# Optimization experiments

Measured on AMD Instinct MI355X. Metric: run time of the kernel, lower is better.

Reference implementation:

```python
import jax, jax.numpy as jnp
import numpy as np

L, B, IN, H, OUT = 4, 4096, 1024, 1024, 1024


def setup_inputs() -> dict:
    key = jax.random.key(0)
    ks = jax.random.split(key, 9)
    std = 1.0 / (H + IN) ** 0.5
    return {
        "x": jax.random.normal(ks[0], (B, IN), jnp.float32),
        "h_prev": jax.random.normal(ks[1], (L, B, H), jnp.float32),
        "c_prev": jax.random.normal(ks[2], (L, B, H), jnp.float32),
        "Wi": jax.random.uniform(ks[3], (L, IN, 4 * H), jnp.float32, -std, std),
        "Wh": jax.random.uniform(ks[4], (L, H, 4 * H), jnp.float32, -std, std),
        "bi": jax.random.uniform(ks[5], (L, 4 * H), jnp.float32, -std, std),
        "bh": jax.random.uniform(ks[6], (L, 4 * H), jnp.float32, -std, std),
        "fc_W": jax.random.uniform(ks[7], (H, OUT), jnp.float32, -std, std),
        "fc_b": jax.random.uniform(ks[8], (OUT,), jnp.float32, -std, std),
    }


def _lstm_cell(x, h, c, Wi, Wh, bi, bh):
    # gates: [B, 4H], split into (input, forget, cell, output)
    gates = x @ Wi + bi + h @ Wh + bh
    i, f, g, o = jnp.split(gates, 4, axis=1)
    i, f, o = jax.nn.sigmoid(i), jax.nn.sigmoid(f), jax.nn.sigmoid(o)
    g = jnp.tanh(g)
    c_cur = f * c + i * g
    h_cur = o * jnp.tanh(c_cur)
    return h_cur, c_cur


def reference(x, h_prev, c_prev, Wi, Wh, bi, bh, fc_W, fc_b):
    h_out, c_out = [], []
    x_in = x
    for l in range(L):  # fixed small layer loop
        h_cur, c_cur = _lstm_cell(x_in, h_prev[l], c_prev[l], Wi[l], Wh[l], bi[l], bh[l])
        h_out.append(h_cur)
        c_out.append(c_cur)
        x_in = h_cur
    h_out = jnp.stack(h_out, axis=0)
    c_out = jnp.stack(c_out, axis=0)
    y = h_out[-1] @ fc_W + fc_b
    return y, h_out, c_out
```

## Files before the change

### kernel.cpp

```cpp
#include <hip/hip_runtime.h>

#define B_    4096
#define H_    1024
#define NLAY  4
#define NT512 512

typedef __attribute__((ext_vector_type(8))) short bf16x8;
typedef __attribute__((ext_vector_type(4))) short s16x4;
typedef __attribute__((ext_vector_type(4))) float f32x4;
typedef unsigned short ushort_t;

__device__ __forceinline__ ushort_t f2bf(float f) {
  unsigned u = __builtin_bit_cast(unsigned, f);
  u += 0x7FFFu + ((u >> 16) & 1u);
  return (ushort_t)(u >> 16);
}

__device__ __forceinline__ float fast_sigmoid(float x) {
  float e = __expf(-fabsf(x));
  float s = 1.0f / (1.0f + e);
  return x >= 0.0f ? s : 1.0f - s;
}
__device__ __forceinline__ float fast_tanh(float x) {
  float e = __expf(-2.0f * fabsf(x));
  float t = (1.0f - e) / (1.0f + e);
  return x >= 0.0f ? t : -t;
}

#define GLDS16(gsrc, ldst)                                                  \
  __builtin_amdgcn_global_load_lds(                                         \
      (__attribute__((address_space(1))) void*)(gsrc),                      \
      (__attribute__((address_space(3))) void*)(ldst), 16, 0, 0)

#define BAR()                                                               \
  { asm volatile("" ::: "memory");                                          \
    __builtin_amdgcn_s_barrier();                                           \
    asm volatile("" ::: "memory"); }

#define WAITV(N)                                                            \
  { asm volatile("s_waitcnt vmcnt(" #N ")" ::: "memory");                   \
    __builtin_amdgcn_sched_barrier(0); }

__global__ __launch_bounds__(NT512, 2) void lstm8(
    const ushort_t* __restrict__ aX, const ushort_t* __restrict__ aH,
    const float* __restrict__ cprev, const float* __restrict__ bi,
    const float* __restrict__ bh, const ushort_t* __restrict__ wt,
    float* __restrict__ hout, float* __restrict__ cout,
    ushort_t* __restrict__ hbfout) {
  __shared__ __align__(16) char sL[131072];

  const int tid  = threadIdx.x;
  const int lane = tid & 63;
  const int wid  = tid >> 6;
  const int wm   = wid >> 2;
  const int wn   = wid & 3;
  const int bid  = (blockIdx.x & 7) * 32 + (blockIdx.x >> 3);
  const int bm   = bid & 15;
  const int bn   = bid >> 4;

  const int fr    = lane & 15;
  const int oF    = lane >> 4;
  const int s_    = oF ^ ((fr >> 1) & 3);
  const int aBase = (wm * 128 + fr) * 64 + s_ * 16;
  const int bBase = (wn * 64 + fr) * 64 + s_ * 16;

  const int rA = tid >> 2;
  const int oA = (tid & 3) ^ ((rA >> 1) & 3);
  const size_t aOff = (size_t)(bm * 256 + rA) * 1024 + oA * 8;

  const ushort_t* wtBn = wt + (size_t)bn * 64 * 8192;

  f32x4 acc[8][4];
#pragma unroll
  for (int m = 0; m < 8; ++m)
#pragma unroll
    for (int g = 0; g < 4; ++g) acc[m][g] = (f32x4){0.f, 0.f, 0.f, 0.f};

#pragma unroll
  for (int t = 0; t < 3; ++t) {
    const ushort_t* s0 = aX + aOff + t * 32;
    GLDS16(s0,          sL + t * 32768 + wid * 1024);
    GLDS16(s0 + 131072, sL + t * 32768 + 8192 + wid * 1024);
    const ushort_t* sb = wtBn + (size_t)t * 8192 + tid * 8;
    GLDS16(sb,        sL + t * 32768 + 16384 + wid * 1024);
    GLDS16(sb + 4096, sL + t * 32768 + 16384 + 8192 + wid * 1024);
  }
  WAITV(8);
  BAR();

#define TSTEP(BUFC, T, ISSUE)                                                \
  {                                                                          \
    const char* pa = sL + (BUFC) * 32768;                                    \
    const char* pb = pa + 16384;                                             \
    char* nbuf = sL + (((BUFC) + 3) & 3) * 32768;                            \
    bf16x8 a[8], b0, b1;                                                     \
    _Pragma("unroll")                                                        \
    for (int m = 0; m < 8; ++m)                                              \
      a[m] = *(const bf16x8*)(pa + aBase + m * 1024);                        \
    b0 = *(const bf16x8*)(pb + bBase);                                       \
    b1 = *(const bf16x8*)(pb + bBase + 1024);                                \
    if (ISSUE) {                                                             \
      const int tt = (T) + 3;                                                \
      const ushort_t* s0 = (tt < 32 ? aX : aH) + (aOff + (tt & 31) * 32);    \
      GLDS16(s0,          nbuf + wid * 1024);                                \
      GLDS16(s0 + 131072, nbuf + 8192 + wid * 1024);                         \
    }                                                                        \
    __builtin_amdgcn_s_setprio(1);                                           \
    _Pragma("unroll")                                                        \
    for (int m = 0; m < 8; ++m)                                              \
      acc[m][0] =                                                            \
          __builtin_amdgcn_mfma_f32_16x16x32_bf16(a[m], b0, acc[m][0], 0, 0, 0); \
    _Pragma("unroll")                                                        \
    for (int m = 0; m < 8; ++m)                                              \
      acc[m][1] =                                                            \
          __builtin_amdgcn_mfma_f32_16x16x32_bf16(a[m], b1, acc[m][1], 0, 0, 0); \
    __builtin_amdgcn_s_setprio(0);                                           \
    bf16x8 b2 = *(const bf16x8*)(pb + bBase + 2048);                         \
    bf16x8 b3 = *(const bf16x8*)(pb + bBase + 3072);                         \
    if (ISSUE) {                                                             \
      const int tt = (T) + 3;                                                \
      const ushort_t* sb = wtBn + (size_t)tt * 8192 + tid * 8;               \
      GLDS16(sb,        nbuf + 16384 + wid * 1024);                          \
      GLDS16(sb + 4096, nbuf + 16384 + 8192 + wid * 1024);                   \
    }                                                                        \
    __builtin_amdgcn_s_setprio(1);                                           \
    _Pragma("unroll")                                                        \
    for (int m = 0; m < 8; ++m)                                              \
      acc[m][2] =                                                            \
          __builtin_amdgcn_mfma_f32_16x16x32_bf16(a[m], b2, acc[m][2], 0, 0, 0); \
    _Pragma("unroll")                                                        \
    for (int m = 0; m < 8; ++m)                                              \
      acc[m][3] =                                                            \
          __builtin_amdgcn_mfma_f32_16x16x32_bf16(a[m], b3, acc[m][3], 0, 0, 0); \
    __builtin_amdgcn_s_setprio(0);                                           \
  }

#pragma unroll 1
  for (int t = 0; t < 60; t += 4) {
    TSTEP(0, t + 0, 1) WAITV(8); BAR();
    TSTEP(1, t + 1, 1) WAITV(8); BAR();
    TSTEP(2, t + 2, 1) WAITV(8); BAR();
    TSTEP(3, t + 3, 1) WAITV(8); BAR();
  }
  TSTEP(0, 60, 1) WAITV(8); BAR();
  TSTEP(1, 61, 0) WAITV(4); BAR();
  TSTEP(2, 62, 0) WAITV(0); BAR();
  TSTEP(3, 63, 0)
#undef TSTEP

  const int hcolL = wn * 16 + fr;
  const int hcol  = bn * 64 + hcolL;
  float bsum[4];
#pragma unroll
  for (int g = 0; g < 4; ++g)
    bsum[g] = bi[g * 1024 + hcol] + bh[g * 1024 + hcol];

#define LSTRIDE 68
  float* LF = (float*)sL;
  const int crow = (tid >> 4);
  const int cc4  = (tid & 15) * 4;
  BAR();
  {
    const float* cp0 = cprev + (size_t)(bm * 256) * 1024 + bn * 64;
#pragma unroll
    for (int i = 0; i < 8; ++i) {
      const int row = i * 32 + crow;
      f32x4 v = *(const f32x4*)(cp0 + (size_t)row * 1024 + cc4);
      *(f32x4*)(LF + row * LSTRIDE + cc4) = v;
    }
  }
  BAR();
  float cv[8][4], hv[8][4];
#pragma unroll
  for (int m = 0; m < 8; ++m) {
    const int rowb = wm * 128 + m * 16 + oF * 4;
#pragma unroll
    for (int r = 0; r < 4; ++r) {
      const float cp = LF[(rowb + r) * LSTRIDE + hcolL];
      const float gi = fast_sigmoid(acc[m][0][r] + bsum[0]);
      const float gf = fast_sigmoid(acc[m][1][r] + bsum[1]);
      const float gg = fast_tanh(acc[m][2][r] + bsum[2]);
      const float go = fast_sigmoid(acc[m][3][r] + bsum[3]);
      const float c  = gf * cp + gi * gg;
      cv[m][r] = c;
      hv[m][r] = go * fast_tanh(c);
    }
  }
  BAR();
#pragma unroll
  for (int m = 0; m < 8; ++m) {
    const int rowb = wm * 128 + m * 16 + oF * 4;
#pragma unroll
    for (int r = 0; r < 4; ++r) LF[(rowb + r) * LSTRIDE + hcolL] = cv[m][r];
  }
  BAR();
  {
    float* co0 = cout + (size_t)(bm * 256) * 1024 + bn * 64;
#pragma unroll
    for (int i = 0; i < 8; ++i) {
      const int row = i * 32 + crow;
      f32x4 v = *(const f32x4*)(LF + row * LSTRIDE + cc4);
      *(f32x4*)(co0 + (size_t)row * 1024 + cc4) = v;
    }
  }
  BAR();
#pragma unroll
  for (int m = 0; m < 8; ++m) {
    const int rowb = wm * 128 + m * 16 + oF * 4;
#pragma unroll
    for (int r = 0; r < 4; ++r) LF[(rowb + r) * LSTRIDE + hcolL] = hv[m][r];
  }
  BAR();
  {
    float* ho0 = hout + (size_t)(bm * 256) * 1024 + bn * 64;
    ushort_t* hb0 = hbfout + (size_t)(bm * 256) * 1024 + bn * 64;
#pragma unroll
    for (int i = 0; i < 8; ++i) {
      const int row = i * 32 + crow;
      f32x4 v = *(const f32x4*)(LF + row * LSTRIDE + cc4);
      *(f32x4*)(ho0 + (size_t)row * 1024 + cc4) = v;
      s16x4 hb;
#pragma unroll
      for (int j = 0; j < 4; ++j) hb[j] = (short)f2bf(v[j]);
      *(s16x4*)(hb0 + (size_t)row * 1024 + cc4) = hb;
    }
  }
#undef LSTRIDE
}

__global__ __launch_bounds__(NT512) void packW(const float* __restrict__ Wi,
                                               const float* __restrict__ Wh,
                                               ushort_t* __restrict__ wt) {
  __shared__ ushort_t t16[64 * 256];
  const int bn = blockIdx.x;
  const int kb = blockIdx.y;
  const int l  = blockIdx.z;
  const int tid = threadIdx.x;
  const int kq = tid >> 6, cc = tid & 63;
  const int k0 = kb * 64;
  const float* W = (k0 < 1024)
                       ? (Wi + (size_t)l * 1024 * 4096 + (size_t)k0 * 4096)
                       : (Wh + (size_t)l * 1024 * 4096 + (size_t)(k0 - 1024) * 4096);
#pragma unroll
  for (int kk = 0; kk < 8; ++kk) {
    const int kl = kq * 8 + kk;
#pragma unroll
    for (int g = 0; g < 4; ++g) {
      const float v = W[(size_t)kl * 4096 + g * 1024 + bn * 64 + cc];
      const int p = (cc >> 4) * 64 + g * 16 + (cc & 15);
      t16[kl * 256 + p] = f2bf(v);
    }
  }
  __syncthreads();
#pragma unroll
  for (int half = 0; half < 2; ++half) {
    ushort_t* tile =
        wt + (((size_t)l * 16 + bn) * 64 + kb * 2 + half) * 8192;
#pragma unroll
    for (int j = 0; j < 2; ++j) {
      const int q = j * 512 + tid;
      const int r = q >> 2, s = q & 3;
      const int o = s ^ ((r >> 1) & 3);
      const int kl = half * 32 + o * 8;
      bf16x8 ov;
#pragma unroll
      for (int i = 0; i < 8; ++i) ov[i] = (short)t16[(kl + i) * 256 + r];
      *(bf16x8*)(tile + (size_t)q * 8) = ov;
    }
  }
}

__device__ __forceinline__ int swz(int row, int kelem) {
  return ((row * 64 + kelem) * 2) ^ ((row & 7) << 4);
}

__global__ __launch_bounds__(NT512) void fc_kernel(
    const ushort_t* __restrict__ wtfc, const ushort_t* __restrict__ abf,
    const float* __restrict__ bias, float* __restrict__ y) {
  __shared__ __align__(16) char sA[128 * 64 * 2];
  __shared__ __align__(16) char sB[64 * 64 * 2];
  const int tid  = threadIdx.x;
  const int lane = tid & 63;
  const int wid  = tid >> 6;
  const int wm   = wid >> 2;
  const int wn   = wid & 3;
  const int bid  = (blockIdx.x & 7) * 64 + (blockIdx.x >> 3);
  const int bm   = bid & 31;
  const int bn   = bid >> 5;

  f32x4 acc[4];
#pragma unroll
  for (int m = 0; m < 4; ++m) acc[m] = (f32x4){0.f, 0.f, 0.f, 0.f};

  const int rloc = wid * 8 + (lane >> 3);
  const int jA   = (lane & 7) ^ ((lane >> 3) & 7);
  const ushort_t* aSrc = abf + (size_t)(bm * 128 + rloc) * 1024 + jA * 8;

  for (int ks = 0; ks < 16; ++ks) {
    __syncthreads();
    GLDS16(wtfc + (size_t)(bn * 16 + ks) * 4096 + tid * 8, sB + wid * 1024);
    const int off = ks * 64;
    GLDS16(aSrc + off,             sA + wid * 1024);
    GLDS16(aSrc + off + 64 * 1024, sA + 8192 + wid * 1024);
    __syncthreads();
#pragma unroll
    for (int kk = 0; kk < 64; kk += 32) {
      const int ke = kk + (lane >> 4) * 8;
      bf16x8 a[4];
#pragma unroll
      for (int m = 0; m < 4; ++m)
        a[m] = *(const bf16x8*)(sA + swz(wm * 64 + m * 16 + (lane & 15), ke));
      bf16x8 b = *(const bf16x8*)(sB + swz(wn * 16 + (lane & 15), ke));
#pragma unroll
      for (int m = 0; m < 4; ++m)
        acc[m] = __builtin_amdgcn_mfma_f32_16x16x32_bf16(a[m], b, acc[m], 0, 0, 0);
    }
  }
  const int col = bn * 64 + wn * 16 + (lane & 15);
  const float bb = bias[col];
#pragma unroll
  for (int m = 0; m < 4; ++m) {
    const int row0 = bm * 128 + wm * 64 + m * 16 + ((lane >> 4) << 2);
#pragma unroll
    for (int r = 0; r < 4; ++r)
      y[(size_t)(row0 + r) * 1024 + col] = acc[m][r] + bb;
  }
}

__global__ __launch_bounds__(NT512) void transposeFc(const float* __restrict__ W,
                                                     ushort_t* __restrict__ wt) {
  const int bn = blockIdx.x;
  const int ks = blockIdx.y;
  const int tid = threadIdx.x;
  const int c  = tid & 63;
  const int ko = (tid >> 6) * 8;
  float v[8];
#pragma unroll
  for (int j = 0; j < 8; ++j)
    v[j] = W[(size_t)(ks * 64 + ko + j) * 1024 + bn * 64 + c];
  bf16x8 o;
#pragma unroll
  for (int j = 0; j < 8; ++j) o[j] = (short)f2bf(v[j]);
  ushort_t* tile = wt + ((size_t)bn * 16 + ks) * 4096;
  *(bf16x8*)((char*)tile + swz(c, ko)) = o;
}

__global__ __launch_bounds__(256) void cvt_bf16(const float* __restrict__ s,
                                                ushort_t* __restrict__ d,
                                                int n8) {
  const int i = blockIdx.x * 256 + threadIdx.x;
  if (i >= n8) return;
  const float* p = s + (size_t)i * 8;
  f32x4 a = ((const f32x4*)p)[0];
  f32x4 b = ((const f32x4*)p)[1];
  bf16x8 o;
#pragma unroll
  for (int j = 0; j < 4; ++j) {
    o[j]     = (short)f2bf(a[j]);
    o[4 + j] = (short)f2bf(b[j]);
  }
  *(bf16x8*)(d + (size_t)i * 8) = o;
}

extern "C" void kernel_launch(void* const* d_in, const int* in_sizes, int n_in,
                              void* d_out, int out_size, void* d_ws,
                              size_t ws_size, hipStream_t stream) {
  const float* x     = (const float*)d_in[0];
  const float* hprev = (const float*)d_in[1];
  const float* cprev = (const float*)d_in[2];
  const float* Wi    = (const float*)d_in[3];
  const float* Wh    = (const float*)d_in[4];
  const float* bi    = (const float*)d_in[5];
  const float* bh    = (const float*)d_in[6];
  const float* fcW   = (const float*)d_in[7];
  const float* fcb   = (const float*)d_in[8];

  float* out = (float*)d_out;
  const size_t BH = (size_t)B_ * H_;
  float* y    = out;
  float* hout = out + BH;
  float* cout = out + 5 * BH;

  const size_t WT_ELEMS = (size_t)4 * 16 * 64 * 8192;
  const size_t FC_ELEMS = (size_t)16 * 16 * 4096;
  ushort_t* wt      = (ushort_t*)d_ws;
  ushort_t* fcwt    = wt + WT_ELEMS;
  ushort_t* xbf     = fcwt + FC_ELEMS;
  ushort_t* hprevbf = xbf + BH;
  ushort_t* houtbf  = hprevbf + 4 * BH;

  dim3 blk(NT512);
  packW<<<dim3(16, 32, 4), blk, 0, stream>>>(Wi, Wh, wt);
  transposeFc<<<dim3(16, 16), blk, 0, stream>>>(fcW, fcwt);
  cvt_bf16<<<dim3((int)(BH / 8 / 256)), dim3(256), 0, stream>>>(x, xbf,
                                                                (int)(BH / 8));
  cvt_bf16<<<dim3((int)(4 * BH / 8 / 256)), dim3(256), 0, stream>>>(
      hprev, hprevbf, (int)(4 * BH / 8));

  for (int l = 0; l < NLAY; ++l) {
    const ushort_t* aX  = (l == 0) ? xbf : (houtbf + (size_t)(l - 1) * BH);
    const ushort_t* wtl = wt + (size_t)l * 16 * 64 * 8192;
    lstm8<<<dim3(256), blk, 0, stream>>>(
        aX, hprevbf + (size_t)l * BH, cprev + (size_t)l * BH, bi + l * 4096,
        bh + l * 4096, wtl, hout + (size_t)l * BH, cout + (size_t)l * BH,
        houtbf + (size_t)l * BH);
  }
  fc_kernel<<<dim3(512), blk, 0, stream>>>(fcwt, houtbf + 3 * BH, fcb, y);
}
```

Measured before the change: 391.6 us.

## Shrink LSTM GEMM tile and stream weight fragments directly into registers

Each LSTM block now runs 256 threads on a 128x64 output tile instead of 512 threads on 256x64, and launches 512 blocks. Shared memory per block drops from 128KB to 32KB. Only the activation tile is staged through LDS; each wave loads its weight fragments straight from global memory into registers, double-buffered two steps ahead, and packW is changed to lay out weights in MFMA-lane order for this. The aim is higher occupancy and less LDS traffic and capacity pressure, at the cost of less A-tile reuse across column tiles and more register use for the prefetched B fragments.

```diff
diff --git a/kernel.cpp b/kernel.cpp
--- a/kernel.cpp
+++ b/kernel.cpp
@@ -3,7 +3,6 @@
 #define B_    4096
 #define H_    1024
 #define NLAY  4
-#define NT512 512
 
 typedef __attribute__((ext_vector_type(8))) short bf16x8;
 typedef __attribute__((ext_vector_type(4))) short s16x4;
@@ -41,34 +40,30 @@
   { asm volatile("s_waitcnt vmcnt(" #N ")" ::: "memory");                   \
     __builtin_amdgcn_sched_barrier(0); }
 
-__global__ __launch_bounds__(NT512, 2) void lstm8(
+__global__ __launch_bounds__(256, 2) void lstm8(
     const ushort_t* __restrict__ aX, const ushort_t* __restrict__ aH,
     const float* __restrict__ cprev, const float* __restrict__ bi,
-    const float* __restrict__ bh, const ushort_t* __restrict__ wt,
+    const float* __restrict__ bh, const ushort_t* __restrict__ wtl,
     float* __restrict__ hout, float* __restrict__ cout,
     ushort_t* __restrict__ hbfout) {
-  __shared__ __align__(16) char sL[131072];
+  __shared__ __align__(16) char sL[32768];
 
   const int tid  = threadIdx.x;
   const int lane = tid & 63;
   const int wid  = tid >> 6;
-  const int wm   = wid >> 2;
-  const int wn   = wid & 3;
-  const int bid  = (blockIdx.x & 7) * 32 + (blockIdx.x >> 3);
-  const int bm   = bid & 15;
-  const int bn   = bid >> 4;
-
-  const int fr    = lane & 15;
-  const int oF    = lane >> 4;
-  const int s_    = oF ^ ((fr >> 1) & 3);
-  const int aBase = (wm * 128 + fr) * 64 + s_ * 16;
-  const int bBase = (wn * 64 + fr) * 64 + s_ * 16;
-
-  const int rA = tid >> 2;
-  const int oA = (tid & 3) ^ ((rA >> 1) & 3);
-  const size_t aOff = (size_t)(bm * 256 + rA) * 1024 + oA * 8;
-
-  const ushort_t* wtBn = wt + (size_t)bn * 64 * 8192;
+  const int bid  = (blockIdx.x & 7) * 64 + (blockIdx.x >> 3);
+  const int bm   = bid & 31;
+  const int bn   = bid >> 5;
+
+  const int fr = lane & 15;
+  const int oF = lane >> 4;
+  const int aBase = fr * 64 + (oF ^ ((fr >> 1) & 3)) * 16;
+
+  const int rowA = tid >> 2;
+  const int oA   = (tid & 3) ^ ((rowA >> 1) & 3);
+  const size_t aOff = (size_t)(bm * 128 + rowA) * 1024 + oA * 8;
+
+  const ushort_t* wtBn = wtl + (size_t)bn * 524288;
 
   f32x4 acc[8][4];
 #pragma unroll
@@ -76,107 +71,105 @@
 #pragma unroll
     for (int g = 0; g < 4; ++g) acc[m][g] = (f32x4){0.f, 0.f, 0.f, 0.f};
 
-#pragma unroll
-  for (int t = 0; t < 3; ++t) {
-    const ushort_t* s0 = aX + aOff + t * 32;
-    GLDS16(s0,          sL + t * 32768 + wid * 1024);
-    GLDS16(s0 + 131072, sL + t * 32768 + 8192 + wid * 1024);
-    const ushort_t* sb = wtBn + (size_t)t * 8192 + tid * 8;
-    GLDS16(sb,        sL + t * 32768 + 16384 + wid * 1024);
-    GLDS16(sb + 4096, sL + t * 32768 + 16384 + 8192 + wid * 1024);
-  }
-  WAITV(8);
-  BAR();
-
-#define TSTEP(BUFC, T, ISSUE)                                                \
+  bf16x8 bs0[4], bs1[4], bs2[4], bs3[4];
+
+#define STAGE_A(NB, T)                                                       \
   {                                                                          \
-    const char* pa = sL + (BUFC) * 32768;                                    \
-    const char* pb = pa + 16384;                                             \
-    char* nbuf = sL + (((BUFC) + 3) & 3) * 32768;                            \
-    bf16x8 a[8], b0, b1;                                                     \
+    const ushort_t* s0 = (((T) < 32) ? aX : aH) + aOff + ((T) & 31) * 32;    \
+    GLDS16(s0,         sL + (NB) * 8192 + wid * 1024);                       \
+    GLDS16(s0 + 65536, sL + (NB) * 8192 + 4096 + wid * 1024);                \
+  }
+#define LOADB(SET, T)                                                        \
+  {                                                                          \
+    const ushort_t* b0 =                                                     \
+        wtBn + ((size_t)(T) * 16 + wid * 4) * 512 + lane * 8;                \
+    SET[0] = *(const bf16x8*)(b0);                                           \
+    SET[1] = *(const bf16x8*)(b0 + 512);                                     \
+    SET[2] = *(const bf16x8*)(b0 + 1024);                                    \
+    SET[3] = *(const bf16x8*)(b0 + 1536);                                    \
+  }
+
+  STAGE_A(0, 0)
+  LOADB(bs0, 0)
+  STAGE_A(1, 1)
+  LOADB(bs1, 1)
+  STAGE_A(2, 2)
+  WAITV(8)
+  BAR()
+
+#define TSTEP(CB, NB, T, BU, BL, IB, IA)                                     \
+  {                                                                          \
+    const char* pa = sL + (CB) * 8192;                                       \
+    bf16x8 a[4];                                                             \
     _Pragma("unroll")                                                        \
-    for (int m = 0; m < 8; ++m)                                              \
+    for (int m = 0; m < 4; ++m)                                              \
       a[m] = *(const bf16x8*)(pa + aBase + m * 1024);                        \
-    b0 = *(const bf16x8*)(pb + bBase);                                       \
-    b1 = *(const bf16x8*)(pb + bBase + 1024);                                \
-    if (ISSUE) {                                                             \
-      const int tt = (T) + 3;                                                \
-      const ushort_t* s0 = (tt < 32 ? aX : aH) + (aOff + (tt & 31) * 32);    \
-      GLDS16(s0,          nbuf + wid * 1024);                                \
-      GLDS16(s0 + 131072, nbuf + 8192 + wid * 1024);                         \
-    }                                                                        \
+    if (IB) LOADB(BL, (T) + 2)                                               \
     __builtin_amdgcn_s_setprio(1);                                           \
     _Pragma("unroll")                                                        \
-    for (int m = 0; m < 8; ++m)                                              \
-      acc[m][0] =                                                            \
-          __builtin_amdgcn_mfma_f32_16x16x32_bf16(a[m], b0, acc[m][0], 0, 0, 0); \
+    for (int g = 0; g < 4; ++g)                                              \
+      _Pragma("unroll")                                                      \
+      for (int m = 0; m < 4; ++m)                                            \
+        acc[m][g] = __builtin_amdgcn_mfma_f32_16x16x32_bf16(a[m], BU[g],     \
+                                                            acc[m][g], 0, 0, 0); \
+    __builtin_amdgcn_s_setprio(0);                                           \
     _Pragma("unroll")                                                        \
-    for (int m = 0; m < 8; ++m)                                              \
-      acc[m][1] =                                                            \
-          __builtin_amdgcn_mfma_f32_16x16x32_bf16(a[m], b1, acc[m][1], 0, 0, 0); \
-    __builtin_amdgcn_s_setprio(0);                                           \
-    bf16x8 b2 = *(const bf16x8*)(pb + bBase + 2048);                         \
-    bf16x8 b3 = *(const bf16x8*)(pb + bBase + 3072);                         \
-    if (ISSUE) {                                                             \
-      const int tt = (T) + 3;                                                \
-      const ushort_t* sb = wtBn + (size_t)tt * 8192 + tid * 8;               \
-      GLDS16(sb,        nbuf + 16384 + wid * 1024);                          \
-      GLDS16(sb + 4096, nbuf + 16384 + 8192 + wid * 1024);                   \
-    }                                                                        \
+    for (int m = 0; m < 4; ++m)                                              \
+      a[m] = *(const bf16x8*)(pa + aBase + 4096 + m * 1024);                 \
+    if (IA) STAGE_A(NB, (T) + 3)                                             \
     __builtin_amdgcn_s_setprio(1);                                           \
     _Pragma("unroll")                                                        \
-    for (int m = 0; m < 8; ++m)                                              \
-      acc[m][2] =                                                            \
-          __builtin_amdgcn_mfma_f32_16x16x32_bf16(a[m], b2, acc[m][2], 0, 0, 0); \
-    _Pragma("unroll")                                                        \
-    for (int m = 0; m < 8; ++m)                                              \
-      acc[m][3] =                                                            \
-          __builtin_amdgcn_mfma_f32_16x16x32_bf16(a[m], b3, acc[m][3], 0, 0, 0); \
+    for (int g = 0; g < 4; ++g)                                              \
+      _Pragma("unroll")                                                      \
+      for (int m = 0; m < 4; ++m)                                            \
+        acc[m + 4][g] = __builtin_amdgcn_mfma_f32_16x16x32_bf16(              \
+            a[m], BU[g], acc[m + 4][g], 0, 0, 0);                            \
     __builtin_amdgcn_s_setprio(0);                                           \
   }
 
 #pragma unroll 1
   for (int t = 0; t < 60; t += 4) {
-    TSTEP(0, t + 0, 1) WAITV(8); BAR();
-    TSTEP(1, t + 1, 1) WAITV(8); BAR();
-    TSTEP(2, t + 2, 1) WAITV(8); BAR();
-    TSTEP(3, t + 3, 1) WAITV(8); BAR();
-  }
-  TSTEP(0, 60, 1) WAITV(8); BAR();
-  TSTEP(1, 61, 0) WAITV(4); BAR();
-  TSTEP(2, 62, 0) WAITV(0); BAR();
-  TSTEP(3, 63, 0)
+    TSTEP(0, 3, t + 0, bs0, bs2, 1, 1) WAITV(8) BAR()
+    TSTEP(1, 0, t + 1, bs1, bs3, 1, 1) WAITV(8) BAR()
+    TSTEP(2, 1, t + 2, bs2, bs0, 1, 1) WAITV(8) BAR()
+    TSTEP(3, 2, t + 3, bs3, bs1, 1, 1) WAITV(8) BAR()
+  }
+  TSTEP(0, 3, 60, bs0, bs2, 1, 1) WAITV(8) BAR()
+  TSTEP(1, 0, 61, bs1, bs3, 1, 0) WAITV(6) BAR()
+  TSTEP(2, 1, 62, bs2, bs0, 0, 0) WAITV(0) BAR()
+  TSTEP(3, 2, 63, bs3, bs0, 0, 0)
 #undef TSTEP
-
-  const int hcolL = wn * 16 + fr;
+#undef STAGE_A
+#undef LOADB
+
+  const int hcolL = wid * 16 + fr;
   const int hcol  = bn * 64 + hcolL;
   float bsum[4];
 #pragma unroll
   for (int g = 0; g < 4; ++g)
     bsum[g] = bi[g * 1024 + hcol] + bh[g * 1024 + hcol];
 
-#define LSTRIDE 68
   float* LF = (float*)sL;
-  const int crow = (tid >> 4);
+  const int crow = tid >> 4;
   const int cc4  = (tid & 15) * 4;
-  BAR();
+  BAR()
   {
-    const float* cp0 = cprev + (size_t)(bm * 256) * 1024 + bn * 64;
+    const float* cp0 = cprev + (size_t)(bm * 128) * 1024 + bn * 64;
 #pragma unroll
     for (int i = 0; i < 8; ++i) {
-      const int row = i * 32 + crow;
+      const int row = i * 16 + crow;
       f32x4 v = *(const f32x4*)(cp0 + (size_t)row * 1024 + cc4);
-      *(f32x4*)(LF + row * LSTRIDE + cc4) = v;
-    }
-  }
-  BAR();
+      *(f32x4*)(LF + row * 64 + cc4) = v;
+    }
+  }
+  BAR()
   float cv[8][4], hv[8][4];
 #pragma unroll
   for (int m = 0; m < 8; ++m) {
-    const int rowb = wm * 128 + m * 16 + oF * 4;
+    const int rowb = m * 16 + oF * 4;
 #pragma unroll
     for (int r = 0; r < 4; ++r) {
-      const float cp = LF[(rowb + r) * LSTRIDE + hcolL];
+      const float cp = LF[(rowb + r) * 64 + hcolL];
       const float gi = fast_sigmoid(acc[m][0][r] + bsum[0]);
       const float gf = fast_sigmoid(acc[m][1][r] + bsum[1]);
       const float gg = fast_tanh(acc[m][2][r] + bsum[2]);
@@ -186,38 +179,38 @@
       hv[m][r] = go * fast_tanh(c);
     }
   }
-  BAR();
+  BAR()
 #pragma unroll
   for (int m = 0; m < 8; ++m) {
-    const int rowb = wm * 128 + m * 16 + oF * 4;
-#pragma unroll
-    for (int r = 0; r < 4; ++r) LF[(rowb + r) * LSTRIDE + hcolL] = cv[m][r];
-  }
-  BAR();
+    const int rowb = m * 16 + oF * 4;
+#pragma unroll
+    for (int r = 0; r < 4; ++r) LF[(rowb + r) * 64 + hcolL] = cv[m][r];
+  }
+  BAR()
   {
-    float* co0 = cout + (size_t)(bm * 256) * 1024 + bn * 64;
+    float* co0 = cout + (size_t)(bm * 128) * 1024 + bn * 64;
 #pragma unroll
     for (int i = 0; i < 8; ++i) {
-      const int row = i * 32 + crow;
-      f32x4 v = *(const f32x4*)(LF + row * LSTRIDE + cc4);
+      const int row = i * 16 + crow;
+      f32x4 v = *(const f32x4*)(LF + row * 64 + cc4);
       *(f32x4*)(co0 + (size_t)row * 1024 + cc4) = v;
     }
   }
-  BAR();
+  BAR()
 #pragma unroll
   for (int m = 0; m < 8; ++m) {
-    const int rowb = wm * 128 + m * 16 + oF * 4;
-#pragma unroll
-    for (int r = 0; r < 4; ++r) LF[(rowb + r) * LSTRIDE + hcolL] = hv[m][r];
-  }
-  BAR();
+    const int rowb = m * 16 + oF * 4;
+#pragma unroll
+    for (int r = 0; r < 4; ++r) LF[(rowb + r) * 64 + hcolL] = hv[m][r];
+  }
+  BAR()
   {
-    float* ho0 = hout + (size_t)(bm * 256) * 1024 + bn * 64;
-    ushort_t* hb0 = hbfout + (size_t)(bm * 256) * 1024 + bn * 64;
+    float* ho0 = hout + (size_t)(bm * 128) * 1024 + bn * 64;
+    ushort_t* hb0 = hbfout + (size_t)(bm * 128) * 1024 + bn * 64;
 #pragma unroll
     for (int i = 0; i < 8; ++i) {
-      const int row = i * 32 + crow;
-      f32x4 v = *(const f32x4*)(LF + row * LSTRIDE + cc4);
+      const int row = i * 16 + crow;
+      f32x4 v = *(const f32x4*)(LF + row * 64 + cc4);
       *(f32x4*)(ho0 + (size_t)row * 1024 + cc4) = v;
       s16x4 hb;
 #pragma unroll
@@ -225,12 +218,11 @@
       *(s16x4*)(hb0 + (size_t)row * 1024 + cc4) = hb;
     }
   }
-#undef LSTRIDE
-}
-
-__global__ __launch_bounds__(NT512) void packW(const float* __restrict__ Wi,
-                                               const float* __restrict__ Wh,
-                                               ushort_t* __restrict__ wt) {
+}
+
+__global__ __launch_bounds__(512) void packW(const float* __restrict__ Wi,
+                                             const float* __restrict__ Wh,
+                                             ushort_t* __restrict__ wt) {
   __shared__ ushort_t t16[64 * 256];
   const int bn = blockIdx.x;
   const int kb = blockIdx.y;
@@ -254,18 +246,18 @@
   __syncthreads();
 #pragma unroll
   for (int half = 0; half < 2; ++half) {
-    ushort_t* tile =
-        wt + (((size_t)l * 16 + bn) * 64 + kb * 2 + half) * 8192;
-#pragma unroll
-    for (int j = 0; j < 2; ++j) {
-      const int q = j * 512 + tid;
-      const int r = q >> 2, s = q & 3;
-      const int o = s ^ ((r >> 1) & 3);
-      const int kl = half * 32 + o * 8;
+    const int kt = kb * 2 + half;
+    ushort_t* tile = wt + (((size_t)l * 16 + bn) * 64 + kt) * 8192;
+#pragma unroll
+    for (int c = 0; c < 2; ++c) {
+      const int idx = c * 512 + tid;
+      const int ln  = idx & 63;
+      const int p   = (idx >> 6) * 16 + (ln & 15);
+      const int klb = half * 32 + (ln >> 4) * 8;
       bf16x8 ov;
 #pragma unroll
-      for (int i = 0; i < 8; ++i) ov[i] = (short)t16[(kl + i) * 256 + r];
-      *(bf16x8*)(tile + (size_t)q * 8) = ov;
+      for (int j = 0; j < 8; ++j) ov[j] = (short)t16[(klb + j) * 256 + p];
+      *(bf16x8*)(tile + (size_t)idx * 8) = ov;
     }
   }
 }
@@ -274,7 +266,7 @@
   return ((row * 64 + kelem) * 2) ^ ((row & 7) << 4);
 }
 
-__global__ __launch_bounds__(NT512) void fc_kernel(
+__global__ __launch_bounds__(512) void fc_kernel(
     const ushort_t* __restrict__ wtfc, const ushort_t* __restrict__ abf,
     const float* __restrict__ bias, float* __restrict__ y) {
   __shared__ __align__(16) char sA[128 * 64 * 2];
@@ -327,8 +319,8 @@
   }
 }
 
-__global__ __launch_bounds__(NT512) void transposeFc(const float* __restrict__ W,
-                                                     ushort_t* __restrict__ wt) {
+__global__ __launch_bounds__(512) void transposeFc(const float* __restrict__ W,
+                                                   ushort_t* __restrict__ wt) {
   const int bn = blockIdx.x;
   const int ks = blockIdx.y;
   const int tid = threadIdx.x;
@@ -389,9 +381,8 @@
   ushort_t* hprevbf = xbf + BH;
   ushort_t* houtbf  = hprevbf + 4 * BH;
 
-  dim3 blk(NT512);
-  packW<<<dim3(16, 32, 4), blk, 0, stream>>>(Wi, Wh, wt);
-  transposeFc<<<dim3(16, 16), blk, 0, stream>>>(fcW, fcwt);
+  packW<<<dim3(16, 32, 4), dim3(512), 0, stream>>>(Wi, Wh, wt);
+  transposeFc<<<dim3(16, 16), dim3(512), 0, stream>>>(fcW, fcwt);
   cvt_bf16<<<dim3((int)(BH / 8 / 256)), dim3(256), 0, stream>>>(x, xbf,
                                                                 (int)(BH / 8));
   cvt_bf16<<<dim3((int)(4 * BH / 8 / 256)), dim3(256), 0, stream>>>(
@@ -400,10 +391,10 @@
   for (int l = 0; l < NLAY; ++l) {
     const ushort_t* aX  = (l == 0) ? xbf : (houtbf + (size_t)(l - 1) * BH);
     const ushort_t* wtl = wt + (size_t)l * 16 * 64 * 8192;
-    lstm8<<<dim3(256), blk, 0, stream>>>(
+    lstm8<<<dim3(512), dim3(256), 0, stream>>>(
         aX, hprevbf + (size_t)l * BH, cprev + (size_t)l * BH, bi + l * 4096,
         bh + l * 4096, wtl, hout + (size_t)l * BH, cout + (size_t)l * BH,
         houtbf + (size_t)l * BH);
   }
-  fc_kernel<<<dim3(512), blk, 0, stream>>>(fcwt, houtbf + 3 * BH, fcb, y);
-}
+  fc_kernel<<<dim3(512), dim3(512), 0, stream>>>(fcwt, houtbf + 3 * BH, fcb, y);
+}
```

New measurement: 431.2 us. 1.1x slower.
